# Kernel tuning notes

Measured on AMD Instinct MI355X. Metric: run time of the kernel, lower is better.

## Reference

```python
import jax, jax.numpy as jnp
import numpy as np
from jax import lax

# Module config (from init_kwargs)
PADDING = (1, 1)
DILATION = (1, 1)
GROUPS = 1
# stride param is initialized to ones(2); effective integer stride = floor(stride) = (1, 1).
# Output shape depends on this value, so it must be static under jit.
INT_STRIDE = (1, 1)


def setup_inputs() -> dict:
    key = jax.random.key(0)
    k1, k2 = jax.random.split(key)
    B, Cin, H, W = 32, 128, 64, 64
    Cout, kH, kW = 256, 3, 3
    x = jax.random.normal(k1, (B, Cin, H, W), dtype=jnp.float32)
    # reset_parameters: uniform(-stdv, stdv), stdv = 1/sqrt(Cin*kH*kW)
    stdv = 1.0 / np.sqrt(Cin * kH * kW)
    weight = jax.random.uniform(k2, (Cout, Cin // GROUPS, kH, kW), dtype=jnp.float32,
                                minval=-stdv, maxval=stdv)
    stride = jnp.ones((2,), dtype=jnp.float32)
    return {"x": x, "weight": weight, "stride": stride}


def reference(x, weight, stride):
    # Integer strides = floor(stride); with stride initialized to ones this is (1, 1).
    # (Static under jit; floor has zero derivative a.e., so stride only affects
    #  sampling locations, exactly as in the CUDA im2col forward.)
    out = lax.conv_general_dilated(
        x, weight,
        window_strides=INT_STRIDE,
        padding=[(PADDING[0], PADDING[0]), (PADDING[1], PADDING[1])],
        rhs_dilation=DILATION,
        dimension_numbers=("NCHW", "OIHW", "NCHW"),
        feature_group_count=GROUPS,
    )
    return out
```

## Files before the change

### kernel.cpp

```cpp
#include <hip/hip_runtime.h>

typedef __attribute__((ext_vector_type(8))) short short8;
typedef __attribute__((ext_vector_type(4))) float f32x4;

#define XP_ELEMS (32u * 66u * 66u * 128u)
#define WT_ELEMS (256u * 1152u)
#define WS_NEED  ((size_t)(XP_ELEMS + WT_ELEMS) * 2u)

typedef const __attribute__((address_space(1))) void* gp1_t;
typedef __attribute__((address_space(3))) void* lp3_t;

__device__ __forceinline__ void gload16(const void* g, void* l) {
  __builtin_amdgcn_global_load_lds((gp1_t)g, (lp3_t)l, 16, 0, 0);
}

__device__ __forceinline__ short f2bf(float f) {
  unsigned u = __float_as_uint(f);
  u = (u + 0x7FFFu + ((u >> 16) & 1u)) >> 16;
  return (short)u;
}

__global__ __launch_bounds__(256) void prepass_x(const float* __restrict__ x,
                                                 short* __restrict__ xp) {
  __shared__ short lds[64 * 128];
  const int y = blockIdx.x;
  const int b = blockIdx.y;
  const int t = threadIdx.x;

  const float* src = x + (long)b * 128 * 4096 + y * 64;
#pragma unroll
  for (int i = 0; i < 8; ++i) {
    int f4 = t + i * 256;
    int cin = f4 >> 4, px4 = f4 & 15;
    float4 v = *(const float4*)(src + (long)cin * 4096 + px4 * 4);
    float vv[4] = {v.x, v.y, v.z, v.w};
#pragma unroll
    for (int j = 0; j < 4; ++j) {
      int px = px4 * 4 + j;
      int g = (cin >> 3) ^ ((px ^ (px >> 2)) & 15);
      lds[px * 128 + (g << 3) + (cin & 7)] = f2bf(vv[j]);
    }
  }
  __syncthreads();
  short* dst = xp + ((long)(b * 66 + y + 1) * 66 + 1) * 128;
#pragma unroll
  for (int i = 0; i < 4; ++i) {
    int f8 = t + i * 256;
    int px = f8 >> 4, c8 = f8 & 15;
    int g = c8 ^ ((px ^ (px >> 2)) & 15);
    short8 v = *(const short8*)&lds[px * 128 + (g << 3)];
    *(short8*)(dst + (long)px * 128 + c8 * 8) = v;
  }
  short8 z = (short8)0;
  short* rowbase = xp + (long)(b * 66 + y + 1) * 66 * 128;
  if (t < 32) {
    int px = (t < 16) ? 0 : 65;
    int c8 = t & 15;
    *(short8*)(rowbase + (long)px * 128 + c8 * 8) = z;
  }
  if (y == 0) {
    short* r0 = xp + (long)(b * 66) * 66 * 128;
    for (int idx = t; idx < 66 * 16; idx += 256) *(short8*)(r0 + idx * 8) = z;
  }
  if (y == 63) {
    short* r65 = xp + ((long)(b * 66) + 65) * 66 * 128;
    for (int idx = t; idx < 66 * 16; idx += 256) *(short8*)(r65 + idx * 8) = z;
  }
}

__global__ __launch_bounds__(256) void prepass_w(const float* __restrict__ w,
                                                 short* __restrict__ wt) {
  int o    = blockIdx.x * 256 + threadIdx.x;
  int cout = o / 1152;
  int r    = o % 1152;
  int kh   = r / 384;
  int kw   = (r / 128) % 3;
  int cin  = r & 127;
  wt[o] = f2bf(w[((cout * 128 + cin) * 3 + kh) * 3 + kw]);
}

__global__ __launch_bounds__(256, 3) void conv_gemm(const short* __restrict__ xp,
                                                    const short* __restrict__ wt,
                                                    float* __restrict__ out) {
  __shared__ alignas(16) short Alds[3 * 128 * 32];
  __shared__ alignas(16) short Blds[3 * 128 * 32];
  const int tid   = threadIdx.x;
  const int w     = tid >> 6;
  const int l     = tid & 63;
  const int l15   = l & 15;
  const int q     = l >> 4;
  const int ntile = blockIdx.x;
  const int m0    = blockIdx.y << 7;

  const int r  = tid >> 2;
  const int p  = tid & 3;
  const int cs = p ^ ((r >> 1) & 3);
  const long aoff0 = (long)(m0 + r) * 1152 + (cs << 3);
  const long aoff1 = aoff0 + (long)64 * 1152;
  long boff0, boff1;
  {
    int n0 = (ntile << 7) + r;
    int bb = n0 >> 12, yy = (n0 >> 6) & 63, xx = n0 & 63;
    boff0 = ((long)(bb * 66 + yy) * 66 + xx) * 128 + (cs << 3);
    int n1 = n0 + 64;
    bb = n1 >> 12; yy = (n1 >> 6) & 63; xx = n1 & 63;
    boff1 = ((long)(bb * 66 + yy) * 66 + xx) * 128 + (cs << 3);
  }
  const int ldst0 = r * 32 + p * 8;
  const int ldst1 = ldst0 + 2048;

  const int wm = (w >> 1) << 6;
  const int wn = (w & 1) << 6;
  int aRd[4], bRd[4];
#pragma unroll
  for (int i = 0; i < 4; ++i) {
    int rA = wm + (i << 4) + l15;
    aRd[i] = rA * 32 + ((q ^ ((rA >> 1) & 3)) << 3);
    int rB = wn + (i << 4) + l15;
    bRd[i] = rB * 32 + ((q ^ ((rB >> 1) & 3)) << 3);
  }

  f32x4 acc[4][4];
#pragma unroll
  for (int i = 0; i < 4; ++i)
#pragma unroll
    for (int j = 0; j < 4; ++j) acc[i][j] = (f32x4)0.f;

  auto STAGE = [&](int slot, int ks) {
    const int kq  = ks >> 2;
    const int kh  = kq / 3, kw2 = kq - kh * 3;
    const int sB  = (kh * 66 + kw2) * 128 + ((ks & 3) << 5);
    const int ka  = ks << 5;
    short* Ad = &Alds[slot * 4096];
    short* Bd = &Blds[slot * 4096];
    gload16(wt + aoff0 + ka, Ad + ldst0);
    gload16(wt + aoff1 + ka, Ad + ldst1);
    gload16(xp + boff0 + sB, Bd + ldst0);
    gload16(xp + boff1 + sB, Bd + ldst1);
  };

  auto COMPUTE = [&](int slot) {
    const short* Ab = &Alds[slot * 4096];
    const short* Bb = &Blds[slot * 4096];
    short8 af[4], bf[4];
#pragma unroll
    for (int i = 0; i < 4; ++i) af[i] = *(const short8*)&Ab[aRd[i]];
#pragma unroll
    for (int j = 0; j < 4; ++j) bf[j] = *(const short8*)&Bb[bRd[j]];
    __builtin_amdgcn_s_setprio(1);
#pragma unroll
    for (int i = 0; i < 4; ++i)
#pragma unroll
      for (int j = 0; j < 4; ++j)
        acc[i][j] = __builtin_amdgcn_mfma_f32_16x16x32_bf16(af[i], bf[j],
                                                            acc[i][j], 0, 0, 0);
    __builtin_amdgcn_s_setprio(0);
  };

#define BAR()   __builtin_amdgcn_s_barrier()
#define VMC(n)  asm volatile("s_waitcnt vmcnt(" #n ")" ::: "memory")

  STAGE(0, 0);
  STAGE(1, 1);
  VMC(4);
  BAR();

  int s_cur = 0, s_nxt = 1, s_stg = 2;
#pragma unroll 1
  for (int ks = 0; ks < 34; ++ks) {
    STAGE(s_stg, ks + 2);
    COMPUTE(s_cur);
    VMC(4);
    BAR();
    int t0 = s_cur; s_cur = s_nxt; s_nxt = s_stg; s_stg = t0;
  }
  COMPUTE(s_cur);
  VMC(0);
  BAR();
  COMPUTE(s_nxt);

  const int ngb = (ntile << 7) + wn;
  const int b   = ngb >> 12;
  const int yxb = ngb & 4095;
  float* outb = out + (long)b * (256 * 4096) + yxb + l15;
#pragma unroll
  for (int i = 0; i < 4; ++i) {
#pragma unroll
    for (int rr = 0; rr < 4; ++rr) {
      const int cout = m0 + wm + (i << 4) + q * 4 + rr;
      float* orow = outb + (long)cout * 4096;
#pragma unroll
      for (int j = 0; j < 4; ++j) orow[j * 16] = acc[i][j][rr];
    }
  }
#undef BAR
#undef VMC
}

__global__ __launch_bounds__(256) void naive_conv(const float* __restrict__ x,
                                                  const float* __restrict__ wgt,
                                                  float* __restrict__ out) {
  long o = (long)blockIdx.x * 256 + threadIdx.x;
  int xx = (int)(o & 63);
  int y  = (int)((o >> 6) & 63);
  int co = (int)((o >> 12) & 255);
  int b  = (int)(o >> 20);
  float s = 0.f;
  for (int ci = 0; ci < 128; ++ci) {
    for (int kh = 0; kh < 3; ++kh) {
      int iy = y + kh - 1;
      if (iy < 0 || iy > 63) continue;
      for (int kw = 0; kw < 3; ++kw) {
        int ix = xx + kw - 1;
        if (ix < 0 || ix > 63) continue;
        s += x[((long)(b * 128 + ci) * 64 + iy) * 64 + ix] *
             wgt[((co * 128 + ci) * 3 + kh) * 3 + kw];
      }
    }
  }
  out[o] = s;
}

extern "C" void kernel_launch(void* const* d_in, const int* in_sizes, int n_in,
                              void* d_out, int out_size, void* d_ws, size_t ws_size,
                              hipStream_t stream) {
  (void)in_sizes; (void)n_in;
  const float* x   = (const float*)d_in[0];
  const float* wgt = (const float*)d_in[1];
  float* out = (float*)d_out;
  if (ws_size >= WS_NEED) {
    short* xp = (short*)d_ws;
    short* wt = xp + XP_ELEMS;
    prepass_x<<<dim3(64, 32), dim3(256), 0, stream>>>(x, xp);
    prepass_w<<<dim3(WT_ELEMS / 256), dim3(256), 0, stream>>>(wgt, wt);
    conv_gemm<<<dim3(1024, 2), dim3(256), 0, stream>>>(xp, wt, out);
  } else {
    naive_conv<<<dim3(out_size / 256), dim3(256), 0, stream>>>(x, wgt, out);
  }
}
```

Measured before the change: 277.6 us.

## Load B operand directly from global into registers with 4-stage A ring and register double-buffering

The input-activation (B) tiles no longer go through LDS. Each lane loads its MFMA fragments straight from global memory into double-buffered registers, while the weight (A) tiles use a 4-slot LDS ring staged three steps ahead. The main loop is unrolled by two and uses explicit lgkmcnt/vmcnt waits and sched barriers so that loads overlap the MFMAs. This removes the B-side LDS writes and reads and halves LDS use, but the B global loads are less coalesced, are repeated across the two waves that share the same columns, and increase register pressure.

After: 333.8 us. +20.2%, slower.

```diff
diff --git a/kernel.cpp b/kernel.cpp
--- a/kernel.cpp
+++ b/kernel.cpp
@@ -9,6 +9,7 @@
 
 typedef const __attribute__((address_space(1))) void* gp1_t;
 typedef __attribute__((address_space(3))) void* lp3_t;
+typedef const __attribute__((address_space(1))) short8* g8p_t;
 
 __device__ __forceinline__ void gload16(const void* g, void* l) {
   __builtin_amdgcn_global_load_lds((gp1_t)g, (lp3_t)l, 16, 0, 0);
@@ -82,8 +83,7 @@
 __global__ __launch_bounds__(256, 3) void conv_gemm(const short* __restrict__ xp,
                                                     const short* __restrict__ wt,
                                                     float* __restrict__ out) {
-  __shared__ alignas(16) short Alds[3 * 128 * 32];
-  __shared__ alignas(16) short Blds[3 * 128 * 32];
+  __shared__ alignas(16) short Alds[4 * 128 * 32];
   const int tid   = threadIdx.x;
   const int w     = tid >> 6;
   const int l     = tid & 63;
@@ -97,28 +97,21 @@
   const int cs = p ^ ((r >> 1) & 3);
   const long aoff0 = (long)(m0 + r) * 1152 + (cs << 3);
   const long aoff1 = aoff0 + (long)64 * 1152;
-  long boff0, boff1;
-  {
-    int n0 = (ntile << 7) + r;
-    int bb = n0 >> 12, yy = (n0 >> 6) & 63, xx = n0 & 63;
-    boff0 = ((long)(bb * 66 + yy) * 66 + xx) * 128 + (cs << 3);
-    int n1 = n0 + 64;
-    bb = n1 >> 12; yy = (n1 >> 6) & 63; xx = n1 & 63;
-    boff1 = ((long)(bb * 66 + yy) * 66 + xx) * 128 + (cs << 3);
-  }
   const int ldst0 = r * 32 + p * 8;
   const int ldst1 = ldst0 + 2048;
 
   const int wm = (w >> 1) << 6;
   const int wn = (w & 1) << 6;
-  int aRd[4], bRd[4];
+  int aRd[4];
 #pragma unroll
   for (int i = 0; i < 4; ++i) {
     int rA = wm + (i << 4) + l15;
     aRd[i] = rA * 32 + ((q ^ ((rA >> 1) & 3)) << 3);
-    int rB = wn + (i << 4) + l15;
-    bRd[i] = rB * 32 + ((q ^ ((rB >> 1) & 3)) << 3);
-  }
+  }
+
+  const int nb  = (ntile << 7) + wn + l15;
+  const int bbi = nb >> 12, byy = (nb >> 6) & 63, bxx = nb & 63;
+  const short* bbase = xp + ((long)(bbi * 66 + byy) * 66 + bxx) * 128 + (q << 3);
 
   f32x4 acc[4][4];
 #pragma unroll
@@ -126,58 +119,89 @@
 #pragma unroll
     for (int j = 0; j < 4; ++j) acc[i][j] = (f32x4)0.f;
 
-  auto STAGE = [&](int slot, int ks) {
-    const int kq  = ks >> 2;
-    const int kh  = kq / 3, kw2 = kq - kh * 3;
-    const int sB  = (kh * 66 + kw2) * 128 + ((ks & 3) << 5);
-    const int ka  = ks << 5;
-    short* Ad = &Alds[slot * 4096];
-    short* Bd = &Blds[slot * 4096];
-    gload16(wt + aoff0 + ka, Ad + ldst0);
-    gload16(wt + aoff1 + ka, Ad + ldst1);
-    gload16(xp + boff0 + sB, Bd + ldst0);
-    gload16(xp + boff1 + sB, Bd + ldst1);
-  };
-
-  auto COMPUTE = [&](int slot) {
-    const short* Ab = &Alds[slot * 4096];
-    const short* Bb = &Blds[slot * 4096];
-    short8 af[4], bf[4];
-#pragma unroll
-    for (int i = 0; i < 4; ++i) af[i] = *(const short8*)&Ab[aRd[i]];
-#pragma unroll
-    for (int j = 0; j < 4; ++j) bf[j] = *(const short8*)&Bb[bRd[j]];
+  short8 aF0[4], aF1[4], bF0[4], bF1[4];
+
+#define BAR()   __builtin_amdgcn_s_barrier()
+#define SBAR()  __builtin_amdgcn_sched_barrier(0)
+#define LGK(n)  asm volatile("s_waitcnt lgkmcnt(" #n ")" ::: "memory")
+#define VMC(n)  asm volatile("s_waitcnt vmcnt(" #n ")" ::: "memory")
+
+  auto STG = [&](int ks) {
+    const int sb = (ks & 3) << 12;
+    gload16(wt + aoff0 + ((long)ks << 5), &Alds[sb + ldst0]);
+    gload16(wt + aoff1 + ((long)ks << 5), &Alds[sb + ldst1]);
+  };
+  auto LDB = [&](int ks, short8 (&bN)[4]) {
+    const int kq = ks >> 2;
+    const int kh = kq / 3, kw2 = kq - kh * 3;
+    const short* bp = bbase + ((kh * 66 + kw2) << 7) + ((ks & 3) << 5);
+#pragma unroll
+    for (int j = 0; j < 4; ++j)
+      bN[j] = *(g8p_t)(bp + j * 2048);
+  };
+  auto ARD = [&](int ks, short8 (&aN)[4]) {
+    const int sb = (ks & 3) << 12;
+#pragma unroll
+    for (int i = 0; i < 4; ++i)
+      aN[i] = *(const short8*)&Alds[sb + aRd[i]];
+  };
+  auto MM = [&](short8 (&aC)[4], short8 (&bC)[4]) {
     __builtin_amdgcn_s_setprio(1);
 #pragma unroll
     for (int i = 0; i < 4; ++i)
 #pragma unroll
       for (int j = 0; j < 4; ++j)
-        acc[i][j] = __builtin_amdgcn_mfma_f32_16x16x32_bf16(af[i], bf[j],
+        acc[i][j] = __builtin_amdgcn_mfma_f32_16x16x32_bf16(aC[i], bC[j],
                                                             acc[i][j], 0, 0, 0);
     __builtin_amdgcn_s_setprio(0);
   };
 
-#define BAR()   __builtin_amdgcn_s_barrier()
-#define VMC(n)  asm volatile("s_waitcnt vmcnt(" #n ")" ::: "memory")
-
-  STAGE(0, 0);
-  STAGE(1, 1);
+  auto BODY = [&](int ks, short8 (&aC)[4], short8 (&aN)[4],
+                          short8 (&bC)[4], short8 (&bN)[4]) {
+    STG(ks + 3);
+    LDB(ks + 1, bN);
+    ARD(ks + 1, aN);
+    LGK(4);
+    VMC(6);
+    SBAR();
+    MM(aC, bC);
+    BAR(); SBAR();
+  };
+
+  STG(0); STG(1); STG(2);
+  LDB(0, bF0);
+  VMC(6);
+  BAR(); SBAR();
+  ARD(0, aF0);
+  LGK(0);
+  SBAR();
+
+#pragma unroll 1
+  for (int it = 0; it < 16; ++it) {
+    const int ks = it << 1;
+    BODY(ks,     aF0, aF1, bF0, bF1);
+    BODY(ks + 1, aF1, aF0, bF1, bF0);
+  }
+  BODY(32, aF0, aF1, bF0, bF1);
+
+  LDB(34, bF0);
+  ARD(34, aF0);
+  LGK(4);
   VMC(4);
-  BAR();
-
-  int s_cur = 0, s_nxt = 1, s_stg = 2;
-#pragma unroll 1
-  for (int ks = 0; ks < 34; ++ks) {
-    STAGE(s_stg, ks + 2);
-    COMPUTE(s_cur);
-    VMC(4);
-    BAR();
-    int t0 = s_cur; s_cur = s_nxt; s_nxt = s_stg; s_stg = t0;
-  }
-  COMPUTE(s_cur);
+  SBAR();
+  MM(aF1, bF1);
+  BAR(); SBAR();
+  LDB(35, bF1);
+  ARD(35, aF1);
+  LGK(4);
+  VMC(4);
+  SBAR();
+  MM(aF0, bF0);
+  BAR(); SBAR();
+  LGK(0);
   VMC(0);
-  BAR();
-  COMPUTE(s_nxt);
+  SBAR();
+  MM(aF1, bF1);
 
   const int ngb = (ntile << 7) + wn;
   const int b   = ngb >> 12;
@@ -194,6 +218,8 @@
     }
   }
 #undef BAR
+#undef SBAR
+#undef LGK
 #undef VMC
 }
 
```
